# Performance work log

Measured on AMD Instinct MI355X. Metric: run time of the kernel, lower is better.

## Reference

```python
import jax, jax.numpy as jnp
import numpy as np

# MANO fingertip / palm prior vertex indices from contact_loss
_F1 = [697,698,699,700,712,713,714,715,737,738,739,740,741,743,744,745,746,748,749,750,753,754,755,756,757,758,759,760,761,762,763,764,765,766,767,768]
_F2 = [46,47,48,49,164,165,166,167,194,195,223,237,238,280,281,298,301,317,320,323,324,325,326,327,328,329,330,331,332,333,340,341,342,343,344,345,346,347,348,349,350,351,352,353,354,355]
_F3 = [356,357,358,359,375,376,386,387,396,397,402,403,413,429,433,434,435,436,437,438,439,440,441,442,443,444,452,453,454,455,456,459,460,461,462,463,464,465,466,467]
_F4 = [468,469,470,471,484,485,486,496,497,506,507,513,514,524,545,546,547,548,549,550,551,552,553,555,563,564,565,566,567,570,572,573,574,575,576,577,578]
_F5 = [580,581,582,583,600,601,602,614,615,624,625,630,631,641,663,664,665,666,667,668,670,672,680,681,682,683,684,686,687,688,689,690,691,692,693,694,695]
_F0 = [73,96,98,99,772,774,775,777]
PRIOR_IDX = np.array(_F1 + _F2 + _F3 + _F4 + _F5 + _F0, dtype=np.int32)

KL_COEF = 0.005
A_W, B_W, C_W, D_W, E_W = 1.0, 0.1, 1000.0, 10.0, 10.0  # init kwargs a..e


def _nn(src, trg):
    """Brute-force 1-NN: src [B,N1,3] -> trg [B,N2,3].
    Returns (sq_dist [B,N1], idx [B,N1], diff src-near [B,N1,3])."""
    d2 = (jnp.sum(src * src, -1)[:, :, None]
          + jnp.sum(trg * trg, -1)[:, None, :]
          - 2.0 * jnp.einsum('bnd,bmd->bnm', src, trg))  # [B,N1,N2]
    idx = jnp.argmin(d2, axis=-1)
    near = jnp.take_along_axis(trg, idx[:, :, None], axis=1)
    diff = src - near
    return jnp.sum(diff * diff, axis=-1), idx, diff


def _p2p_signed(x, y, x_normals):
    """point2point_signed(x, y, x_normals): signed dist y->x, unsigned x->y."""
    _, yidx, y2x = _nn(y, x)  # nearest x for each y
    y_nn_normal = jnp.take_along_axis(x_normals, yidx[:, :, None], axis=1)
    in_out = jnp.sign(jnp.sum(y_nn_normal * y2x, axis=-1))
    y2x_signed = jnp.sqrt(jnp.sum(y2x * y2x, axis=-1)) * in_out  # [B,P2]
    _, _, x2y = _nn(x, y)  # nearest y for each x
    x2y_dist = jnp.sqrt(jnp.sum(x2y * x2y, axis=-1))  # [B,P1]
    return y2x_signed, x2y_dist


def _forward(recon_xyz, gt_xyz, recon_normals, gt_normals, obj_xyz, mean, log_var, v_weights):
    B = recon_xyz.shape[0]
    f32 = recon_xyz.dtype
    # --- CVAE recon (L2) + KLD ---
    recon_loss = jnp.sum((recon_xyz - gt_xyz) ** 2) / B
    kld = -0.5 * jnp.sum(1.0 + log_var - mean ** 2 - jnp.exp(log_var)) / B * 10.0
    # --- obj -> hand NN (squared dists, pytorch3d knn_points convention) ---
    recon_d2, recon_idx, _ = _nn(obj_xyz, recon_xyz)  # [B,3000]
    gt_d2, _, _ = _nn(obj_xyz, gt_xyz)
    # --- contact map from GT NN dist thresholding ---
    cmap = jnp.sqrt(gt_d2) < 0.005  # [B,3000] bool
    # --- contact_loss: obj NN to prior (fingertip/palm) recon verts ---
    prior = recon_xyz[:, PRIOR_IDX, :]
    obj_cd, _, _ = _nn(obj_xyz, prior)
    n_pts = jnp.sum(cmap.astype(f32))
    contact = 3000.0 * jnp.where(n_pts > 0, jnp.sum(obj_cd * cmap) / (B * n_pts), 0.0)
    # --- CMap_consistency_loss ---
    recon_cmap = jnp.sqrt(recon_d2) < 0.005
    consistency = -5.0 * jnp.sum((recon_cmap & cmap).astype(f32)) / (n_pts + 1e-4)
    # --- inter_penetr_loss: interior obj points via NN-normal dot sign ---
    nn_hand = jnp.take_along_axis(recon_xyz, recon_idx[:, :, None], axis=1)
    nn_normal = jnp.take_along_axis(recon_normals, recon_idx[:, :, None], axis=1)
    interior = jnp.sum((nn_hand - obj_xyz) * nn_normal, axis=-1) > 0
    penetr = 100.0 * jnp.sum(recon_d2 * interior) / B
    # --- loss_cnet: signed chamfer consistency ---
    vw2 = v_weights ** (1.0 / 2.5)
    o2h, h2o = _p2p_signed(recon_xyz, obj_xyz, recon_normals)
    o2h_gt, h2o_gt = _p2p_signed(gt_xyz, obj_xyz, gt_normals)
    w_dist = (o2h_gt < 0.01) & (o2h_gt > -0.005)
    w_neg = o2h < 0.0
    w = jnp.where(w_neg, 1.5, jnp.where(w_dist, 1.0, 0.1))
    loss_h = 35.0 * (1.0 - KL_COEF) * jnp.mean(jnp.abs(jnp.abs(h2o) - jnp.abs(h2o_gt)) * vw2)
    loss_o = 30.0 * (1.0 - KL_COEF) * jnp.mean(jnp.abs(o2h - o2h_gt) * w)
    cnet = loss_h + loss_o
    return (A_W * recon_loss + B_W * kld + C_W * penetr
            + D_W * contact + E_W * consistency + cnet)


def setup_inputs() -> dict:
    key = jax.random.key(0)
    ks = jax.random.split(key, 8)
    B, NH, NO, Z = 32, 778, 3000, 64
    s = 0.05  # meter-scale point clouds so contact thresholds (5mm) are meaningful
    def unit(k, shape):
        v = jax.random.normal(k, shape, dtype=jnp.float32)
        return v / jnp.linalg.norm(v, axis=-1, keepdims=True)
    return {
        'recon_xyz': jax.random.normal(ks[0], (B, NH, 3), dtype=jnp.float32) * s,
        'gt_xyz': jax.random.normal(ks[1], (B, NH, 3), dtype=jnp.float32) * s,
        'recon_normals': unit(ks[2], (B, NH, 3)),
        'gt_normals': unit(ks[3], (B, NH, 3)),
        'obj_xyz': jax.random.normal(ks[4], (B, NO, 3), dtype=jnp.float32) * s,
        'mean': jax.random.normal(ks[5], (B, Z), dtype=jnp.float32),
        'log_var': jax.random.normal(ks[6], (B, Z), dtype=jnp.float32) * 0.1,
        'v_weights': jax.random.uniform(ks[7], (NH,), dtype=jnp.float32),
    }


def reference(recon_xyz, gt_xyz, recon_normals, gt_normals, obj_xyz, mean, log_var, v_weights):
    return _forward(recon_xyz, gt_xyz, recon_normals, gt_normals, obj_xyz, mean, log_var, v_weights)
```

## Files before the change

### kernel.cpp

```cpp
#include <hip/hip_runtime.h>
#include <math.h>


#define NB 32
#define NH 778
#define NO 3000
#define NZ 64
#define NP 204
#define JHALF 389
#define OBJ_TILES 12
#define OC_NUM 6
#define OC_SIZE 500

typedef unsigned int uint32;
typedef unsigned long long ull;

__device__ __constant__ int c_prior[NP] = {
  697,698,699,700,712,713,714,715,737,738,739,740,741,743,744,745,746,748,749,750,
  753,754,755,756,757,758,759,760,761,762,763,764,765,766,767,768,
  46,47,48,49,164,165,166,167,194,195,223,237,238,280,281,298,301,317,320,323,
  324,325,326,327,328,329,330,331,332,333,340,341,342,343,344,345,346,347,348,349,
  350,351,352,353,354,355,
  356,357,358,359,375,376,386,387,396,397,402,403,413,429,433,434,435,436,437,438,
  439,440,441,442,443,444,452,453,454,455,456,459,460,461,462,463,464,465,466,467,
  468,469,470,471,484,485,486,496,497,506,507,513,514,524,545,546,547,548,549,550,
  551,552,553,555,563,564,565,566,567,570,572,573,574,575,576,577,578,
  580,581,582,583,600,601,602,614,615,624,625,630,631,641,663,664,665,666,667,668,
  670,672,680,681,682,683,684,686,687,688,689,690,691,692,693,694,695,
  73,96,98,99,772,774,775,777
};

__device__ inline float wave_sum(float v) {
  v += __shfl_down(v, 32);
  v += __shfl_down(v, 16);
  v += __shfl_down(v, 8);
  v += __shfl_down(v, 4);
  v += __shfl_down(v, 2);
  v += __shfl_down(v, 1);
  return v;
}

#define N_MINH (2 * NB * NH)
#define N_PACK (2 * NB * NO)

__global__ void init_kernel(float* accs, uint32* minH, ull* packO) {
  int t = blockIdx.x * blockDim.x + threadIdx.x;
  if (t < 8) accs[t] = 0.0f;
  if (t < N_MINH) minH[t] = 0x7F800000u;
  if (t < N_PACK) packO[t] = ~0ull;
}

__global__ __launch_bounds__(256) void mega1(
    const float* __restrict__ recon, const float* __restrict__ gt,
    const float* __restrict__ obj,
    uint32* __restrict__ minHR, uint32* __restrict__ minHG,
    ull* __restrict__ packR, ull* __restrict__ packG)
{
  const int bid = blockIdx.x;
  const int tid = threadIdx.x;

  if (bid < NB * OBJ_TILES * 2) {
    __shared__ float4 sR[JHALF];
    __shared__ float4 sG[JHALF];
    const int half = bid & 1;
    const int tile = (bid >> 1) % OBJ_TILES;
    const int b = bid / (OBJ_TILES * 2);
    const int jbase = half * JHALF;

    for (int i = tid; i < JHALF; i += 256) {
      const float* p = recon + ((size_t)b * NH + jbase + i) * 3;
      float x = p[0], y = p[1], z = p[2];
      sR[i] = make_float4(x, y, z, x*x + y*y + z*z);
      const float* q = gt + ((size_t)b * NH + jbase + i) * 3;
      float gx = q[0], gy = q[1], gz = q[2];
      sG[i] = make_float4(gx, gy, gz, gx*gx + gy*gy + gz*gz);
    }
    __syncthreads();

    const int o = tile * 256 + tid;
    if (o >= NO) return;
    const float* op = obj + ((size_t)b * NO + o) * 3;
    const float ox = op[0], oy = op[1], oz = op[2];
    const float nx = -2.f * ox, ny = -2.f * oy, nz = -2.f * oz;
    const float o2 = ox*ox + oy*oy + oz*oz;

    float bR = 3.4e38f, bG = 3.4e38f;
    int iR = jbase, iG = jbase;
    for (int i = 0; i < JHALF; ++i) {
      float4 h = sR[i];
      float t = fmaf(nx, h.x, h.w);
      t = fmaf(ny, h.y, t);
      t = fmaf(nz, h.z, t);
      if (t < bR) { bR = t; iR = jbase + i; }
      float4 g = sG[i];
      float u = fmaf(nx, g.x, g.w);
      u = fmaf(ny, g.y, u);
      u = fmaf(nz, g.z, u);
      if (u < bG) { bG = u; iG = jbase + i; }
    }
    float d2R = fmaxf(bR + o2, 0.f);
    float d2G = fmaxf(bG + o2, 0.f);
    const size_t base = (size_t)b * NO + o;
    atomicMin(&packR[base], ((ull)__float_as_uint(d2R) << 32) | (uint32)iR);
    atomicMin(&packG[base], ((ull)__float_as_uint(d2G) << 32) | (uint32)iG);
  } else {
    __shared__ float4 sO[OC_SIZE];
    const int bid2 = bid - NB * OBJ_TILES * 2;
    const int oc = bid2 % OC_NUM;
    const int pt = (bid2 / OC_NUM) % 4;
    const int b = bid2 / (OC_NUM * 4);

    const float* Ob = obj + ((size_t)b * NO + oc * OC_SIZE) * 3;
    for (int i = tid; i < OC_SIZE; i += 256) {
      float x = Ob[3*i], y = Ob[3*i+1], z = Ob[3*i+2];
      sO[i] = make_float4(x, y, z, x*x + y*y + z*z);
    }
    __syncthreads();

    const int j = pt * 256 + tid;
    if (j >= NH) return;
    const float* rp = recon + ((size_t)b * NH + j) * 3;
    const float* gp = gt    + ((size_t)b * NH + j) * 3;
    const float rx = rp[0], ry = rp[1], rz = rp[2];
    const float gx = gp[0], gy = gp[1], gz = gp[2];
    const float nrx = -2.f * rx, nry = -2.f * ry, nrz = -2.f * rz;
    const float ngx = -2.f * gx, ngy = -2.f * gy, ngz = -2.f * gz;
    const float r2 = rx*rx + ry*ry + rz*rz;
    const float g2 = gx*gx + gy*gy + gz*gz;

    float mR = 3.4e38f, mG = 3.4e38f;
    for (int k = 0; k < OC_SIZE; ++k) {
      float4 o4 = sO[k];
      float t = fmaf(nrx, o4.x, o4.w);
      t = fmaf(nry, o4.y, t);
      t = fmaf(nrz, o4.z, t);
      mR = fminf(mR, t);
      float u = fmaf(ngx, o4.x, o4.w);
      u = fmaf(ngy, o4.y, u);
      u = fmaf(ngz, o4.z, u);
      mG = fminf(mG, u);
    }
    float d2R = fmaxf(mR + r2, 0.f);
    float d2G = fmaxf(mG + g2, 0.f);
    const int base = b * NH + j;
    atomicMin(&minHR[base], __float_as_uint(d2R));
    atomicMin(&minHG[base], __float_as_uint(d2G));
  }
}

__global__ __launch_bounds__(256) void mega2(
    const float* __restrict__ recon, const float* __restrict__ gt,
    const float* __restrict__ rnorm, const float* __restrict__ gnorm,
    const float* __restrict__ obj,
    const float* __restrict__ mean, const float* __restrict__ logv,
    const float* __restrict__ vw,
    const uint32* __restrict__ minHR, const uint32* __restrict__ minHG,
    const ull* __restrict__ packR, const ull* __restrict__ packG,
    float* __restrict__ accs)
{
  __shared__ float4 sP[NP];
  __shared__ float red[4][5];
  const int bid = blockIdx.x;
  const int tid = threadIdx.x;
  const int lane = tid & 63, wv = tid >> 6;

  if (bid < NB * OBJ_TILES) {
    const int b = bid / OBJ_TILES;
    const int tile = bid % OBJ_TILES;
    if (tid < NP) {
      int j = c_prior[tid];
      const float* p = recon + ((size_t)b * NH + j) * 3;
      float x = p[0], y = p[1], z = p[2];
      sP[tid] = make_float4(x, y, z, x*x + y*y + z*z);
    }
    __syncthreads();

    const int o = tile * 256 + tid;
    float penetr = 0.f, nptsv = 0.f, contactv = 0.f, consistv = 0.f, lossov = 0.f;
    if (o < NO) {
      const float* op = obj + ((size_t)b * NO + o) * 3;
      const float ox = op[0], oy = op[1], oz = op[2];
      const float nx = -2.f * ox, ny = -2.f * oy, nz = -2.f * oz;
      const float o2 = ox*ox + oy*oy + oz*oz;

      const size_t base = (size_t)b * NO + o;
      ull pR = packR[base], pG = packG[base];
      float d2R = __uint_as_float((uint32)(pR >> 32));
      float d2G = __uint_as_float((uint32)(pG >> 32));
      int idxR = (int)(uint32)pR, idxG = (int)(uint32)pG;

      float bP = 3.4e38f;
      for (int k = 0; k < NP; ++k) {
        float4 h = sP[k];
        float t = fmaf(nx, h.x, h.w);
        t = fmaf(ny, h.y, t);
        t = fmaf(nz, h.z, t);
        bP = fminf(bP, t);
      }
      float d2P = fmaxf(bP + o2, 0.f);

      const float* hR = recon + ((size_t)b * NH + idxR) * 3;
      const float* nR = rnorm + ((size_t)b * NH + idxR) * 3;
      float dotR = (ox - hR[0]) * nR[0] + (oy - hR[1]) * nR[1] + (oz - hR[2]) * nR[2];
      const float* hG = gt + ((size_t)b * NH + idxG) * 3;
      const float* nG = gnorm + ((size_t)b * NH + idxG) * 3;
      float dotG = (ox - hG[0]) * nG[0] + (oy - hG[1]) * nG[1] + (oz - hG[2]) * nG[2];

      float sgnR = (dotR > 0.f) ? 1.f : ((dotR < 0.f) ? -1.f : 0.f);
      float sgnG = (dotG > 0.f) ? 1.f : ((dotG < 0.f) ? -1.f : 0.f);
      float sR_ = sqrtf(d2R), sG_ = sqrtf(d2G);
      float o2h = sR_ * sgnR;
      float o2hg = sG_ * sgnG;

      bool interior = dotR < 0.f;
      bool cmap = sG_ < 0.005f;
      bool rcmap = sR_ < 0.005f;

      penetr   = interior ? d2R : 0.f;
      nptsv    = cmap ? 1.f : 0.f;
      contactv = cmap ? d2P : 0.f;
      consistv = (cmap && rcmap) ? 1.f : 0.f;
      float w = (o2h < 0.f) ? 1.5f
              : (((o2hg < 0.01f) && (o2hg > -0.005f)) ? 1.f : 0.1f);
      lossov = fabsf(o2h - o2hg) * w;
    }
    float vals[5] = {penetr, nptsv, contactv, consistv, lossov};
    for (int q = 0; q < 5; ++q) {
      float s = wave_sum(vals[q]);
      if (lane == 0) red[wv][q] = s;
    }
    __syncthreads();
    if (tid < 5) {
      float s = red[0][tid] + red[1][tid] + red[2][tid] + red[3][tid];
      atomicAdd(&accs[tid], s);
    }
  } else {
    const int t = (bid - NB * OBJ_TILES) * 256 + tid;
    float lossh = 0.f, rsum = 0.f, ksum = 0.f;
    if (t < NB * NH) {
      const float* rp = recon + (size_t)t * 3;
      const float* gp = gt + (size_t)t * 3;
      float d0 = rp[0] - gp[0], d1 = rp[1] - gp[1], d2 = rp[2] - gp[2];
      rsum = d0*d0 + d1*d1 + d2*d2;
      int j = t % NH;
      float h2o  = sqrtf(__uint_as_float(minHR[t]));
      float h2og = sqrtf(__uint_as_float(minHG[t]));
      lossh = fabsf(h2o - h2og) * powf(vw[j], 0.4f);
    }
    if (t < NB * NZ) {
      float m = mean[t], lv = logv[t];
      ksum = 1.f + lv - m * m - expf(lv);
    }
    float vals[3] = {lossh, rsum, ksum};
    for (int q = 0; q < 3; ++q) {
      float s = wave_sum(vals[q]);
      if (lane == 0) red[wv][q] = s;
    }
    __syncthreads();
    if (tid < 3) {
      float s = red[0][tid] + red[1][tid] + red[2][tid] + red[3][tid];
      atomicAdd(&accs[5 + tid], s);
    }
  }
}

__global__ void final_kernel(const float* __restrict__ a, float* __restrict__ out) {
  const float recon_loss = a[6] / (float)NB;
  const float kld = -0.5f * a[7] / (float)NB * 10.f;
  const float penetr = 100.f * a[0] / (float)NB;
  const float npts = a[1];
  const float contact = (npts > 0.f) ? (3000.f * a[2] / ((float)NB * npts)) : 0.f;
  const float consistency = -5.f * a[3] / (npts + 0.0001f);
  const float lossh = 35.f * (1.f - 0.005f) * (a[5] / (float)(NB * NH));
  const float losso = 30.f * (1.f - 0.005f) * (a[4] / (float)(NB * NO));
  out[0] = recon_loss + 0.1f * kld + 1000.f * penetr + 10.f * contact
         + 10.f * consistency + lossh + losso;
}

__global__ __launch_bounds__(256) void obj_mono(
    const float* __restrict__ recon, const float* __restrict__ gt,
    const float* __restrict__ rnorm, const float* __restrict__ gnorm,
    const float* __restrict__ obj, float* __restrict__ accs)
{
  __shared__ float4 sR[NH];
  __shared__ float4 sG[NH];
  __shared__ float red[4][5];
  const int b = blockIdx.x / OBJ_TILES;
  const int tile = blockIdx.x % OBJ_TILES;
  const int tid = threadIdx.x;

  for (int i = tid; i < NH; i += 256) {
    const float* p = recon + ((size_t)b * NH + i) * 3;
    float x = p[0], y = p[1], z = p[2];
    sR[i] = make_float4(x, y, z, x*x + y*y + z*z);
    const float* q = gt + ((size_t)b * NH + i) * 3;
    float gx = q[0], gy = q[1], gz = q[2];
    sG[i] = make_float4(gx, gy, gz, gx*gx + gy*gy + gz*gz);
  }
  __syncthreads();

  const int o = tile * 256 + tid;
  float penetr = 0.f, nptsv = 0.f, contactv = 0.f, consistv = 0.f, lossov = 0.f;
  if (o < NO) {
    const float* op = obj + ((size_t)b * NO + o) * 3;
    const float ox = op[0], oy = op[1], oz = op[2];
    const float nx = -2.f * ox, ny = -2.f * oy, nz = -2.f * oz;
    const float o2 = ox*ox + oy*oy + oz*oz;
    float bR = 3.4e38f, bG = 3.4e38f;
    int iR = 0, iG = 0;
    for (int i = 0; i < NH; ++i) {
      float4 h = sR[i];
      float t = fmaf(nx, h.x, h.w); t = fmaf(ny, h.y, t); t = fmaf(nz, h.z, t);
      if (t < bR) { bR = t; iR = i; }
      float4 g = sG[i];
      float u = fmaf(nx, g.x, g.w); u = fmaf(ny, g.y, u); u = fmaf(nz, g.z, u);
      if (u < bG) { bG = u; iG = i; }
    }
    float bP = 3.4e38f;
    for (int k = 0; k < NP; ++k) {
      float4 h = sR[c_prior[k]];
      float t = fmaf(nx, h.x, h.w); t = fmaf(ny, h.y, t); t = fmaf(nz, h.z, t);
      bP = fminf(bP, t);
    }
    float d2R = fmaxf(bR + o2, 0.f);
    float d2G = fmaxf(bG + o2, 0.f);
    float d2P = fmaxf(bP + o2, 0.f);
    float4 hR = sR[iR];
    const float* nR = rnorm + ((size_t)b * NH + iR) * 3;
    float dotR = (ox - hR.x) * nR[0] + (oy - hR.y) * nR[1] + (oz - hR.z) * nR[2];
    float4 hG = sG[iG];
    const float* nG = gnorm + ((size_t)b * NH + iG) * 3;
    float dotG = (ox - hG.x) * nG[0] + (oy - hG.y) * nG[1] + (oz - hG.z) * nG[2];
    float sgnR = (dotR > 0.f) ? 1.f : ((dotR < 0.f) ? -1.f : 0.f);
    float sgnG = (dotG > 0.f) ? 1.f : ((dotG < 0.f) ? -1.f : 0.f);
    float sR_ = sqrtf(d2R), sG_ = sqrtf(d2G);
    float o2h = sR_ * sgnR, o2hg = sG_ * sgnG;
    bool interior = dotR < 0.f;
    bool cmap = sG_ < 0.005f, rcmap = sR_ < 0.005f;
    penetr = interior ? d2R : 0.f;
    nptsv = cmap ? 1.f : 0.f;
    contactv = cmap ? d2P : 0.f;
    consistv = (cmap && rcmap) ? 1.f : 0.f;
    float w = (o2h < 0.f) ? 1.5f : (((o2hg < 0.01f) && (o2hg > -0.005f)) ? 1.f : 0.1f);
    lossov = fabsf(o2h - o2hg) * w;
  }
  float vals[5] = {penetr, nptsv, contactv, consistv, lossov};
  const int lane = tid & 63, wv = tid >> 6;
  for (int q = 0; q < 5; ++q) {
    float s = wave_sum(vals[q]);
    if (lane == 0) red[wv][q] = s;
  }
  __syncthreads();
  if (tid < 5) {
    float s = red[0][tid] + red[1][tid] + red[2][tid] + red[3][tid];
    atomicAdd(&accs[tid], s);
  }
}

__global__ __launch_bounds__(256) void hand_full(
    const float* __restrict__ recon, const float* __restrict__ gt,
    const float* __restrict__ obj, const float* __restrict__ vw,
    float* __restrict__ accs)
{
  __shared__ float4 sO[OC_SIZE];
  __shared__ float red[4];
  const int b = blockIdx.x >> 2;
  const int j = ((blockIdx.x & 3) << 8) + threadIdx.x;
  const bool valid = j < NH;
  float rx = 0, ry = 0, rz = 0, gx = 0, gy = 0, gz = 0;
  if (valid) {
    const float* rp = recon + ((size_t)b * NH + j) * 3;
    const float* gp = gt + ((size_t)b * NH + j) * 3;
    rx = rp[0]; ry = rp[1]; rz = rp[2];
    gx = gp[0]; gy = gp[1]; gz = gp[2];
  }
  const float nrx = -2.f*rx, nry = -2.f*ry, nrz = -2.f*rz;
  const float ngx = -2.f*gx, ngy = -2.f*gy, ngz = -2.f*gz;
  const float r2 = rx*rx + ry*ry + rz*rz, g2 = gx*gx + gy*gy + gz*gz;
  float mR = 3.4e38f, mG = 3.4e38f;
  for (int oc = 0; oc < OC_NUM; ++oc) {
    __syncthreads();
    const float* Ob = obj + ((size_t)b * NO + oc * OC_SIZE) * 3;
    for (int i = threadIdx.x; i < OC_SIZE; i += 256) {
      float x = Ob[3*i], y = Ob[3*i+1], z = Ob[3*i+2];
      sO[i] = make_float4(x, y, z, x*x + y*y + z*z);
    }
    __syncthreads();
    if (valid) {
      for (int k = 0; k < OC_SIZE; ++k) {
        float4 o4 = sO[k];
        float t = fmaf(nrx, o4.x, o4.w); t = fmaf(nry, o4.y, t); t = fmaf(nrz, o4.z, t);
        mR = fminf(mR, t);
        float u = fmaf(ngx, o4.x, o4.w); u = fmaf(ngy, o4.y, u); u = fmaf(ngz, o4.z, u);
        mG = fminf(mG, u);
      }
    }
  }
  float lossh = valid ? fabsf(sqrtf(fmaxf(mR + r2, 0.f)) - sqrtf(fmaxf(mG + g2, 0.f)))
                        * powf(vw[j], 0.4f) : 0.f;
  const int lane = threadIdx.x & 63, wv = threadIdx.x >> 6;
  float s = wave_sum(lossh);
  if (lane == 0) red[wv] = s;
  __syncthreads();
  if (threadIdx.x == 0) atomicAdd(&accs[5], red[0] + red[1] + red[2] + red[3]);
}

__global__ __launch_bounds__(256) void tail_nomins(
    const float* __restrict__ recon, const float* __restrict__ gt,
    const float* __restrict__ mean, const float* __restrict__ logv,
    float* __restrict__ accs)
{
  __shared__ float red[4][2];
  const int t = blockIdx.x * 256 + threadIdx.x;
  float rsum = 0.f, ksum = 0.f;
  if (t < NB * NH) {
    const float* rp = recon + (size_t)t * 3;
    const float* gp = gt + (size_t)t * 3;
    float d0 = rp[0] - gp[0], d1 = rp[1] - gp[1], d2 = rp[2] - gp[2];
    rsum = d0*d0 + d1*d1 + d2*d2;
  }
  if (t < NB * NZ) {
    float m = mean[t], lv = logv[t];
    ksum = 1.f + lv - m * m - expf(lv);
  }
  float vals[2] = {rsum, ksum};
  const int lane = threadIdx.x & 63, wv = threadIdx.x >> 6;
  for (int q = 0; q < 2; ++q) {
    float s = wave_sum(vals[q]);
    if (lane == 0) red[wv][q] = s;
  }
  __syncthreads();
  if (threadIdx.x < 2) {
    float s = red[0][threadIdx.x] + red[1][threadIdx.x] + red[2][threadIdx.x] + red[3][threadIdx.x];
    atomicAdd(&accs[6 + threadIdx.x], s);
  }
}

__global__ void init_small(float* accs) {
  int t = threadIdx.x;
  if (t < 8) accs[t] = 0.0f;
}

extern "C" void kernel_launch(void* const* d_in, const int* in_sizes, int n_in,
                              void* d_out, int out_size, void* d_ws, size_t ws_size,
                              hipStream_t stream) {
  const float* recon = (const float*)d_in[0];
  const float* gt    = (const float*)d_in[1];
  const float* rnorm = (const float*)d_in[2];
  const float* gnorm = (const float*)d_in[3];
  const float* obj   = (const float*)d_in[4];
  const float* mean  = (const float*)d_in[5];
  const float* logv  = (const float*)d_in[6];
  const float* vw    = (const float*)d_in[7];
  float* out = (float*)d_out;

  float* accs = (float*)d_ws;
  uint32* minH = (uint32*)(accs + 8);
  ull* packO = (ull*)(minH + N_MINH);
  const size_t needed = 8 * sizeof(float) + (size_t)N_MINH * 4 + (size_t)N_PACK * 8;

  if (ws_size >= needed) {
    {
      int total = N_PACK;
      int blocks = (total + 255) / 256;
      init_kernel<<<blocks, 256, 0, stream>>>(accs, minH, packO);
    }
    mega1<<<NB * OBJ_TILES * 2 + NB * 4 * OC_NUM, 256, 0, stream>>>(
        recon, gt, obj, minH, minH + NB * NH, packO, packO + NB * NO);
    mega2<<<NB * OBJ_TILES + (NB * NH + 255) / 256, 256, 0, stream>>>(
        recon, gt, rnorm, gnorm, obj, mean, logv, vw,
        minH, minH + NB * NH, packO, packO + NB * NO, accs);
    final_kernel<<<1, 1, 0, stream>>>(accs, out);
  } else {
    init_small<<<1, 64, 0, stream>>>(accs);
    obj_mono<<<NB * OBJ_TILES, 256, 0, stream>>>(recon, gt, rnorm, gnorm, obj, accs);
    hand_full<<<NB * 4, 256, 0, stream>>>(recon, gt, obj, vw, accs);
    tail_nomins<<<(NB * NH + 255) / 256, 256, 0, stream>>>(recon, gt, mean, logv, accs);
    final_kernel<<<1, 1, 0, stream>>>(accs, out);
  }
}
```

Measured before the change: 132.2 us.

## Register-block multiple points per thread in NN search and fuse final reduction

```diff
diff --git a/kernel.cpp b/kernel.cpp
--- a/kernel.cpp
+++ b/kernel.cpp
@@ -7,10 +7,20 @@
 #define NO 3000
 #define NZ 64
 #define NP 204
-#define JHALF 389
-#define OBJ_TILES 12
-#define OC_NUM 6
-#define OC_SIZE 500
+
+#define P_OBJ 4
+#define OBJ_PTS (256 * P_OBJ)
+#define OBJ_TILES 3
+#define JSPLIT 4
+#define JCH 195
+#define OC_NUM 12
+#define OC_SIZE 250
+
+#define OBJ_BLKS (NB * OBJ_TILES * JSPLIT)
+#define HAND_BLKS (NB * OC_NUM)
+#define FIN_OBJ_BLKS (NB * OBJ_TILES)
+#define FIN_TAIL_BLKS ((NB * NH + 255) / 256)
+#define FIN_BLKS (FIN_OBJ_BLKS + FIN_TAIL_BLKS)
 
 typedef unsigned int uint32;
 typedef unsigned long long ull;
@@ -45,7 +55,7 @@
 
 __global__ void init_kernel(float* accs, uint32* minH, ull* packO) {
   int t = blockIdx.x * blockDim.x + threadIdx.x;
-  if (t < 8) accs[t] = 0.0f;
+  if (t < 9) accs[t] = 0.0f;
   if (t < N_MINH) minH[t] = 0x7F800000u;
   if (t < N_PACK) packO[t] = ~0ull;
 }
@@ -59,15 +69,17 @@
   const int bid = blockIdx.x;
   const int tid = threadIdx.x;
 
-  if (bid < NB * OBJ_TILES * 2) {
-    __shared__ float4 sR[JHALF];
-    __shared__ float4 sG[JHALF];
-    const int half = bid & 1;
-    const int tile = (bid >> 1) % OBJ_TILES;
-    const int b = bid / (OBJ_TILES * 2);
-    const int jbase = half * JHALF;
-
-    for (int i = tid; i < JHALF; i += 256) {
+  if (bid < OBJ_BLKS) {
+    __shared__ float4 sR[JCH];
+    __shared__ float4 sG[JCH];
+    const int b    = bid / (OBJ_TILES * JSPLIT);
+    const int rem  = bid % (OBJ_TILES * JSPLIT);
+    const int tile = rem / JSPLIT;
+    const int half = rem % JSPLIT;
+    const int jbase = half * JCH;
+    const int jcnt = (NH - jbase < JCH) ? (NH - jbase) : JCH;
+
+    for (int i = tid; i < jcnt; i += 256) {
       const float* p = recon + ((size_t)b * NH + jbase + i) * 3;
       float x = p[0], y = p[1], z = p[2];
       sR[i] = make_float4(x, y, z, x*x + y*y + z*z);
@@ -77,38 +89,59 @@
     }
     __syncthreads();
 
-    const int o = tile * 256 + tid;
-    if (o >= NO) return;
-    const float* op = obj + ((size_t)b * NO + o) * 3;
-    const float ox = op[0], oy = op[1], oz = op[2];
-    const float nx = -2.f * ox, ny = -2.f * oy, nz = -2.f * oz;
-    const float o2 = ox*ox + oy*oy + oz*oz;
-
-    float bR = 3.4e38f, bG = 3.4e38f;
-    int iR = jbase, iG = jbase;
-    for (int i = 0; i < JHALF; ++i) {
+    float nx[P_OBJ], ny[P_OBJ], nz[P_OBJ], o2v[P_OBJ];
+    int ob[P_OBJ]; bool val[P_OBJ];
+    #pragma unroll
+    for (int m = 0; m < P_OBJ; ++m) {
+      int o = tile * OBJ_PTS + m * 256 + tid;
+      ob[m] = o; val[m] = (o < NO);
+      float x = 0.f, y = 0.f, z = 0.f;
+      if (val[m]) {
+        const float* op = obj + ((size_t)b * NO + o) * 3;
+        x = op[0]; y = op[1]; z = op[2];
+      }
+      nx[m] = -2.f * x; ny[m] = -2.f * y; nz[m] = -2.f * z;
+      o2v[m] = x*x + y*y + z*z;
+    }
+
+    float bR[P_OBJ], bG[P_OBJ]; int iR[P_OBJ], iG[P_OBJ];
+    #pragma unroll
+    for (int m = 0; m < P_OBJ; ++m) { bR[m] = 3.4e38f; bG[m] = 3.4e38f; iR[m] = 0; iG[m] = 0; }
+
+    #pragma unroll 2
+    for (int i = 0; i < jcnt; ++i) {
       float4 h = sR[i];
-      float t = fmaf(nx, h.x, h.w);
-      t = fmaf(ny, h.y, t);
-      t = fmaf(nz, h.z, t);
-      if (t < bR) { bR = t; iR = jbase + i; }
+      #pragma unroll
+      for (int m = 0; m < P_OBJ; ++m) {
+        float t = fmaf(nx[m], h.x, h.w);
+        t = fmaf(ny[m], h.y, t);
+        t = fmaf(nz[m], h.z, t);
+        if (t < bR[m]) { bR[m] = t; iR[m] = jbase + i; }
+      }
       float4 g = sG[i];
-      float u = fmaf(nx, g.x, g.w);
-      u = fmaf(ny, g.y, u);
-      u = fmaf(nz, g.z, u);
-      if (u < bG) { bG = u; iG = jbase + i; }
-    }
-    float d2R = fmaxf(bR + o2, 0.f);
-    float d2G = fmaxf(bG + o2, 0.f);
-    const size_t base = (size_t)b * NO + o;
-    atomicMin(&packR[base], ((ull)__float_as_uint(d2R) << 32) | (uint32)iR);
-    atomicMin(&packG[base], ((ull)__float_as_uint(d2G) << 32) | (uint32)iG);
+      #pragma unroll
+      for (int m = 0; m < P_OBJ; ++m) {
+        float u = fmaf(nx[m], g.x, g.w);
+        u = fmaf(ny[m], g.y, u);
+        u = fmaf(nz[m], g.z, u);
+        if (u < bG[m]) { bG[m] = u; iG[m] = jbase + i; }
+      }
+    }
+
+    #pragma unroll
+    for (int m = 0; m < P_OBJ; ++m) {
+      if (!val[m]) continue;
+      const size_t base = (size_t)b * NO + ob[m];
+      float d2R = fmaxf(bR[m] + o2v[m], 0.f);
+      float d2G = fmaxf(bG[m] + o2v[m], 0.f);
+      atomicMin(&packR[base], ((ull)__float_as_uint(d2R) << 32) | (uint32)iR[m]);
+      atomicMin(&packG[base], ((ull)__float_as_uint(d2G) << 32) | (uint32)iG[m]);
+    }
   } else {
     __shared__ float4 sO[OC_SIZE];
-    const int bid2 = bid - NB * OBJ_TILES * 2;
+    const int bid2 = bid - OBJ_BLKS;
     const int oc = bid2 % OC_NUM;
-    const int pt = (bid2 / OC_NUM) % 4;
-    const int b = bid2 / (OC_NUM * 4);
+    const int b  = bid2 / OC_NUM;
 
     const float* Ob = obj + ((size_t)b * NO + oc * OC_SIZE) * 3;
     for (int i = tid; i < OC_SIZE; i += 256) {
@@ -117,34 +150,56 @@
     }
     __syncthreads();
 
-    const int j = pt * 256 + tid;
-    if (j >= NH) return;
-    const float* rp = recon + ((size_t)b * NH + j) * 3;
-    const float* gp = gt    + ((size_t)b * NH + j) * 3;
-    const float rx = rp[0], ry = rp[1], rz = rp[2];
-    const float gx = gp[0], gy = gp[1], gz = gp[2];
-    const float nrx = -2.f * rx, nry = -2.f * ry, nrz = -2.f * rz;
-    const float ngx = -2.f * gx, ngy = -2.f * gy, ngz = -2.f * gz;
-    const float r2 = rx*rx + ry*ry + rz*rz;
-    const float g2 = gx*gx + gy*gy + gz*gz;
-
-    float mR = 3.4e38f, mG = 3.4e38f;
+    float nrx[4], nry[4], nrz[4], r2v[4];
+    float ngx[4], ngy[4], ngz[4], g2v[4];
+    bool val[4];
+    #pragma unroll
+    for (int m = 0; m < 4; ++m) {
+      int j = m * 256 + tid;
+      val[m] = (j < NH);
+      float rx = 0.f, ry = 0.f, rz = 0.f, gx = 0.f, gy = 0.f, gz = 0.f;
+      if (val[m]) {
+        const float* rp = recon + ((size_t)b * NH + j) * 3;
+        const float* gp = gt    + ((size_t)b * NH + j) * 3;
+        rx = rp[0]; ry = rp[1]; rz = rp[2];
+        gx = gp[0]; gy = gp[1]; gz = gp[2];
+      }
+      nrx[m] = -2.f*rx; nry[m] = -2.f*ry; nrz[m] = -2.f*rz;
+      ngx[m] = -2.f*gx; ngy[m] = -2.f*gy; ngz[m] = -2.f*gz;
+      r2v[m] = rx*rx + ry*ry + rz*rz;
+      g2v[m] = gx*gx + gy*gy + gz*gz;
+    }
+
+    float mR[4], mG[4];
+    #pragma unroll
+    for (int m = 0; m < 4; ++m) { mR[m] = 3.4e38f; mG[m] = 3.4e38f; }
+
+    #pragma unroll 2
     for (int k = 0; k < OC_SIZE; ++k) {
       float4 o4 = sO[k];
-      float t = fmaf(nrx, o4.x, o4.w);
-      t = fmaf(nry, o4.y, t);
-      t = fmaf(nrz, o4.z, t);
-      mR = fminf(mR, t);
-      float u = fmaf(ngx, o4.x, o4.w);
-      u = fmaf(ngy, o4.y, u);
-      u = fmaf(ngz, o4.z, u);
-      mG = fminf(mG, u);
-    }
-    float d2R = fmaxf(mR + r2, 0.f);
-    float d2G = fmaxf(mG + g2, 0.f);
-    const int base = b * NH + j;
-    atomicMin(&minHR[base], __float_as_uint(d2R));
-    atomicMin(&minHG[base], __float_as_uint(d2G));
+      #pragma unroll
+      for (int m = 0; m < 4; ++m) {
+        float t = fmaf(nrx[m], o4.x, o4.w);
+        t = fmaf(nry[m], o4.y, t);
+        t = fmaf(nrz[m], o4.z, t);
+        mR[m] = fminf(mR[m], t);
+        float u = fmaf(ngx[m], o4.x, o4.w);
+        u = fmaf(ngy[m], o4.y, u);
+        u = fmaf(ngz[m], o4.z, u);
+        mG[m] = fminf(mG[m], u);
+      }
+    }
+
+    #pragma unroll
+    for (int m = 0; m < 4; ++m) {
+      if (!val[m]) continue;
+      int j = m * 256 + tid;
+      const int base = b * NH + j;
+      float d2R = fmaxf(mR[m] + r2v[m], 0.f);
+      float d2G = fmaxf(mG[m] + g2v[m], 0.f);
+      atomicMin(&minHR[base], __float_as_uint(d2R));
+      atomicMin(&minHG[base], __float_as_uint(d2G));
+    }
   }
 }
 
@@ -156,7 +211,7 @@
     const float* __restrict__ vw,
     const uint32* __restrict__ minHR, const uint32* __restrict__ minHG,
     const ull* __restrict__ packR, const ull* __restrict__ packG,
-    float* __restrict__ accs)
+    float* __restrict__ accs, float* __restrict__ out)
 {
   __shared__ float4 sP[NP];
   __shared__ float red[4][5];
@@ -164,7 +219,7 @@
   const int tid = threadIdx.x;
   const int lane = tid & 63, wv = tid >> 6;
 
-  if (bid < NB * OBJ_TILES) {
+  if (bid < FIN_OBJ_BLKS) {
     const int b = bid / OBJ_TILES;
     const int tile = bid % OBJ_TILES;
     if (tid < NP) {
@@ -175,55 +230,74 @@
     }
     __syncthreads();
 
-    const int o = tile * 256 + tid;
+    float nx[P_OBJ], ny[P_OBJ], nz[P_OBJ], o2v[P_OBJ];
+    float oxv[P_OBJ], oyv[P_OBJ], ozv[P_OBJ];
+    int ob[P_OBJ]; bool val[P_OBJ];
+    #pragma unroll
+    for (int m = 0; m < P_OBJ; ++m) {
+      int o = tile * OBJ_PTS + m * 256 + tid;
+      ob[m] = o; val[m] = (o < NO);
+      float x = 0.f, y = 0.f, z = 0.f;
+      if (val[m]) {
+        const float* op = obj + ((size_t)b * NO + o) * 3;
+        x = op[0]; y = op[1]; z = op[2];
+      }
+      oxv[m] = x; oyv[m] = y; ozv[m] = z;
+      nx[m] = -2.f * x; ny[m] = -2.f * y; nz[m] = -2.f * z;
+      o2v[m] = x*x + y*y + z*z;
+    }
+
+    float bP[P_OBJ];
+    #pragma unroll
+    for (int m = 0; m < P_OBJ; ++m) bP[m] = 3.4e38f;
+    #pragma unroll 2
+    for (int k = 0; k < NP; ++k) {
+      float4 h = sP[k];
+      #pragma unroll
+      for (int m = 0; m < P_OBJ; ++m) {
+        float t = fmaf(nx[m], h.x, h.w);
+        t = fmaf(ny[m], h.y, t);
+        t = fmaf(nz[m], h.z, t);
+        bP[m] = fminf(bP[m], t);
+      }
+    }
+
     float penetr = 0.f, nptsv = 0.f, contactv = 0.f, consistv = 0.f, lossov = 0.f;
-    if (o < NO) {
-      const float* op = obj + ((size_t)b * NO + o) * 3;
-      const float ox = op[0], oy = op[1], oz = op[2];
-      const float nx = -2.f * ox, ny = -2.f * oy, nz = -2.f * oz;
-      const float o2 = ox*ox + oy*oy + oz*oz;
-
-      const size_t base = (size_t)b * NO + o;
+    #pragma unroll
+    for (int m = 0; m < P_OBJ; ++m) {
+      if (!val[m]) continue;
+      const size_t base = (size_t)b * NO + ob[m];
       ull pR = packR[base], pG = packG[base];
       float d2R = __uint_as_float((uint32)(pR >> 32));
       float d2G = __uint_as_float((uint32)(pG >> 32));
       int idxR = (int)(uint32)pR, idxG = (int)(uint32)pG;
-
-      float bP = 3.4e38f;
-      for (int k = 0; k < NP; ++k) {
-        float4 h = sP[k];
-        float t = fmaf(nx, h.x, h.w);
-        t = fmaf(ny, h.y, t);
-        t = fmaf(nz, h.z, t);
-        bP = fminf(bP, t);
-      }
-      float d2P = fmaxf(bP + o2, 0.f);
+      float d2P = fmaxf(bP[m] + o2v[m], 0.f);
 
       const float* hR = recon + ((size_t)b * NH + idxR) * 3;
       const float* nR = rnorm + ((size_t)b * NH + idxR) * 3;
-      float dotR = (ox - hR[0]) * nR[0] + (oy - hR[1]) * nR[1] + (oz - hR[2]) * nR[2];
+      float dotR = (oxv[m] - hR[0]) * nR[0] + (oyv[m] - hR[1]) * nR[1] + (ozv[m] - hR[2]) * nR[2];
       const float* hG = gt + ((size_t)b * NH + idxG) * 3;
       const float* nG = gnorm + ((size_t)b * NH + idxG) * 3;
-      float dotG = (ox - hG[0]) * nG[0] + (oy - hG[1]) * nG[1] + (oz - hG[2]) * nG[2];
+      float dotG = (oxv[m] - hG[0]) * nG[0] + (oyv[m] - hG[1]) * nG[1] + (ozv[m] - hG[2]) * nG[2];
 
       float sgnR = (dotR > 0.f) ? 1.f : ((dotR < 0.f) ? -1.f : 0.f);
       float sgnG = (dotG > 0.f) ? 1.f : ((dotG < 0.f) ? -1.f : 0.f);
       float sR_ = sqrtf(d2R), sG_ = sqrtf(d2G);
-      float o2h = sR_ * sgnR;
-      float o2hg = sG_ * sgnG;
+      float o2h = sR_ * sgnR, o2hg = sG_ * sgnG;
 
       bool interior = dotR < 0.f;
       bool cmap = sG_ < 0.005f;
       bool rcmap = sR_ < 0.005f;
 
-      penetr   = interior ? d2R : 0.f;
-      nptsv    = cmap ? 1.f : 0.f;
-      contactv = cmap ? d2P : 0.f;
-      consistv = (cmap && rcmap) ? 1.f : 0.f;
+      penetr   += interior ? d2R : 0.f;
+      nptsv    += cmap ? 1.f : 0.f;
+      contactv += cmap ? d2P : 0.f;
+      consistv += (cmap && rcmap) ? 1.f : 0.f;
       float w = (o2h < 0.f) ? 1.5f
               : (((o2hg < 0.01f) && (o2hg > -0.005f)) ? 1.f : 0.1f);
-      lossov = fabsf(o2h - o2hg) * w;
-    }
+      lossov += fabsf(o2h - o2hg) * w;
+    }
+
     float vals[5] = {penetr, nptsv, contactv, consistv, lossov};
     for (int q = 0; q < 5; ++q) {
       float s = wave_sum(vals[q]);
@@ -235,7 +309,7 @@
       atomicAdd(&accs[tid], s);
     }
   } else {
-    const int t = (bid - NB * OBJ_TILES) * 256 + tid;
+    const int t = (bid - FIN_OBJ_BLKS) * 256 + tid;
     float lossh = 0.f, rsum = 0.f, ksum = 0.f;
     if (t < NB * NH) {
       const float* rp = recon + (size_t)t * 3;
@@ -262,21 +336,30 @@
       atomicAdd(&accs[5 + tid], s);
     }
   }
-}
-
-__global__ void final_kernel(const float* __restrict__ a, float* __restrict__ out) {
-  const float recon_loss = a[6] / (float)NB;
-  const float kld = -0.5f * a[7] / (float)NB * 10.f;
-  const float penetr = 100.f * a[0] / (float)NB;
-  const float npts = a[1];
-  const float contact = (npts > 0.f) ? (3000.f * a[2] / ((float)NB * npts)) : 0.f;
-  const float consistency = -5.f * a[3] / (npts + 0.0001f);
-  const float lossh = 35.f * (1.f - 0.005f) * (a[5] / (float)(NB * NH));
-  const float losso = 30.f * (1.f - 0.005f) * (a[4] / (float)(NB * NO));
-  out[0] = recon_loss + 0.1f * kld + 1000.f * penetr + 10.f * contact
-         + 10.f * consistency + lossh + losso;
-}
-
+
+  __syncthreads();
+  if (tid == 0) {
+    __threadfence();
+    int* cnt = (int*)(accs + 8);
+    int old = atomicAdd(cnt, 1);
+    if (old == FIN_BLKS - 1) {
+      float a[8];
+      for (int q = 0; q < 8; ++q) a[q] = atomicAdd(&accs[q], 0.0f);
+      const float recon_loss = a[6] / (float)NB;
+      const float kld = -0.5f * a[7] / (float)NB * 10.f;
+      const float penetr = 100.f * a[0] / (float)NB;
+      const float npts = a[1];
+      const float contact = (npts > 0.f) ? (3000.f * a[2] / ((float)NB * npts)) : 0.f;
+      const float consistency = -5.f * a[3] / (npts + 0.0001f);
+      const float lossh = 35.f * (1.f - 0.005f) * (a[5] / (float)(NB * NH));
+      const float losso = 30.f * (1.f - 0.005f) * (a[4] / (float)(NB * NO));
+      out[0] = recon_loss + 0.1f * kld + 1000.f * penetr + 10.f * contact
+             + 10.f * consistency + lossh + losso;
+    }
+  }
+}
+
+#define FB_TILES 12
 __global__ __launch_bounds__(256) void obj_mono(
     const float* __restrict__ recon, const float* __restrict__ gt,
     const float* __restrict__ rnorm, const float* __restrict__ gnorm,
@@ -285,8 +368,8 @@
   __shared__ float4 sR[NH];
   __shared__ float4 sG[NH];
   __shared__ float red[4][5];
-  const int b = blockIdx.x / OBJ_TILES;
-  const int tile = blockIdx.x % OBJ_TILES;
+  const int b = blockIdx.x / FB_TILES;
+  const int tile = blockIdx.x % FB_TILES;
   const int tid = threadIdx.x;
 
   for (int i = tid; i < NH; i += 256) {
@@ -362,7 +445,7 @@
     const float* __restrict__ obj, const float* __restrict__ vw,
     float* __restrict__ accs)
 {
-  __shared__ float4 sO[OC_SIZE];
+  __shared__ float4 sO[500];
   __shared__ float red[4];
   const int b = blockIdx.x >> 2;
   const int j = ((blockIdx.x & 3) << 8) + threadIdx.x;
@@ -378,16 +461,16 @@
   const float ngx = -2.f*gx, ngy = -2.f*gy, ngz = -2.f*gz;
   const float r2 = rx*rx + ry*ry + rz*rz, g2 = gx*gx + gy*gy + gz*gz;
   float mR = 3.4e38f, mG = 3.4e38f;
-  for (int oc = 0; oc < OC_NUM; ++oc) {
-    __syncthreads();
-    const float* Ob = obj + ((size_t)b * NO + oc * OC_SIZE) * 3;
-    for (int i = threadIdx.x; i < OC_SIZE; i += 256) {
+  for (int oc = 0; oc < 6; ++oc) {
+    __syncthreads();
+    const float* Ob = obj + ((size_t)b * NO + oc * 500) * 3;
+    for (int i = threadIdx.x; i < 500; i += 256) {
       float x = Ob[3*i], y = Ob[3*i+1], z = Ob[3*i+2];
       sO[i] = make_float4(x, y, z, x*x + y*y + z*z);
     }
     __syncthreads();
     if (valid) {
-      for (int k = 0; k < OC_SIZE; ++k) {
+      for (int k = 0; k < 500; ++k) {
         float4 o4 = sO[k];
         float t = fmaf(nrx, o4.x, o4.w); t = fmaf(nry, o4.y, t); t = fmaf(nrz, o4.z, t);
         mR = fminf(mR, t);
@@ -441,6 +524,19 @@
   if (t < 8) accs[t] = 0.0f;
 }
 
+__global__ void final_fb(const float* __restrict__ a, float* __restrict__ out) {
+  const float recon_loss = a[6] / (float)NB;
+  const float kld = -0.5f * a[7] / (float)NB * 10.f;
+  const float penetr = 100.f * a[0] / (float)NB;
+  const float npts = a[1];
+  const float contact = (npts > 0.f) ? (3000.f * a[2] / ((float)NB * npts)) : 0.f;
+  const float consistency = -5.f * a[3] / (npts + 0.0001f);
+  const float lossh = 35.f * (1.f - 0.005f) * (a[5] / (float)(NB * NH));
+  const float losso = 30.f * (1.f - 0.005f) * (a[4] / (float)(NB * NO));
+  out[0] = recon_loss + 0.1f * kld + 1000.f * penetr + 10.f * contact
+         + 10.f * consistency + lossh + losso;
+}
+
 extern "C" void kernel_launch(void* const* d_in, const int* in_sizes, int n_in,
                               void* d_out, int out_size, void* d_ws, size_t ws_size,
                               hipStream_t stream) {
@@ -455,27 +551,25 @@
   float* out = (float*)d_out;
 
   float* accs = (float*)d_ws;
-  uint32* minH = (uint32*)(accs + 8);
+  uint32* minH = (uint32*)(accs + 16);
   ull* packO = (ull*)(minH + N_MINH);
-  const size_t needed = 8 * sizeof(float) + (size_t)N_MINH * 4 + (size_t)N_PACK * 8;
+  const size_t needed = 16 * sizeof(float) + (size_t)N_MINH * 4 + (size_t)N_PACK * 8;
 
   if (ws_size >= needed) {
     {
-      int total = N_PACK;
-      int blocks = (total + 255) / 256;
+      int blocks = (N_PACK + 255) / 256;
       init_kernel<<<blocks, 256, 0, stream>>>(accs, minH, packO);
     }
-    mega1<<<NB * OBJ_TILES * 2 + NB * 4 * OC_NUM, 256, 0, stream>>>(
+    mega1<<<OBJ_BLKS + HAND_BLKS, 256, 0, stream>>>(
         recon, gt, obj, minH, minH + NB * NH, packO, packO + NB * NO);
-    mega2<<<NB * OBJ_TILES + (NB * NH + 255) / 256, 256, 0, stream>>>(
+    mega2<<<FIN_BLKS, 256, 0, stream>>>(
         recon, gt, rnorm, gnorm, obj, mean, logv, vw,
-        minH, minH + NB * NH, packO, packO + NB * NO, accs);
-    final_kernel<<<1, 1, 0, stream>>>(accs, out);
+        minH, minH + NB * NH, packO, packO + NB * NO, accs, out);
   } else {
     init_small<<<1, 64, 0, stream>>>(accs);
-    obj_mono<<<NB * OBJ_TILES, 256, 0, stream>>>(recon, gt, rnorm, gnorm, obj, accs);
+    obj_mono<<<NB * FB_TILES, 256, 0, stream>>>(recon, gt, rnorm, gnorm, obj, accs);
     hand_full<<<NB * 4, 256, 0, stream>>>(recon, gt, obj, vw, accs);
     tail_nomins<<<(NB * NH + 255) / 256, 256, 0, stream>>>(recon, gt, mean, logv, accs);
-    final_kernel<<<1, 1, 0, stream>>>(accs, out);
-  }
-}
+    final_fb<<<1, 1, 0, stream>>>(accs, out);
+  }
+}
```

Result: faster. 129.5 us (-2.1%).
